# Optimization experiments

Measured on AMD Instinct MI355X. Metric: run time of the kernel, lower is better.

## Reference

```python
import jax, jax.numpy as jnp
import numpy as np


def _lstm_cell(x, h, c, Wih, Whh, b):
    # torch gate order: input, forget, cell(g), output
    gates = x @ Wih.T + h @ Whh.T + b  # [B, 4H]
    i, f, g, o = jnp.split(gates, 4, axis=-1)
    i = jax.nn.sigmoid(i)
    f = jax.nn.sigmoid(f)
    g = jnp.tanh(g)
    o = jax.nn.sigmoid(o)
    c = f * c + i * g
    return o * jnp.tanh(c), c


def setup_inputs() -> dict:
    key = jax.random.key(0)
    ks = jax.random.split(key, 20)
    B, Te, Td, X, H = 4096, 168, 24, 8, 64
    s = 0.1  # weight scale for numerical sanity in the AR sampling loop
    return {
        "enc_x": jax.random.normal(ks[0], (B, Te, X), jnp.float32),
        "enc_z": jax.random.uniform(ks[1], (B, Te, 1), jnp.float32),
        "dec_x": jax.random.normal(ks[2], (B, Td, X - 1), jnp.float32),
        "v": jax.random.uniform(ks[3], (B, 1, 1), jnp.float32) + 0.5,  # positive scale
        "eps": jax.random.normal(ks[4], (B, Td, 1), jnp.float32),
        "W_ih0": s * jax.random.normal(ks[5], (4 * H, X), jnp.float32),
        "W_hh0": s * jax.random.normal(ks[6], (4 * H, H), jnp.float32),
        "b0": s * jax.random.normal(ks[7], (4 * H,), jnp.float32),
        "W_ih1": s * jax.random.normal(ks[8], (4 * H, H), jnp.float32),
        "W_hh1": s * jax.random.normal(ks[9], (4 * H, H), jnp.float32),
        "b1": s * jax.random.normal(ks[10], (4 * H,), jnp.float32),
        "W_ih2": s * jax.random.normal(ks[11], (4 * H, H), jnp.float32),
        "W_hh2": s * jax.random.normal(ks[12], (4 * H, H), jnp.float32),
        "b2": s * jax.random.normal(ks[13], (4 * H,), jnp.float32),
        "w_m": s * jax.random.normal(ks[14], (H, 1), jnp.float32),
        "b_m": jnp.zeros((1,), jnp.float32),
        "w_a": s * jax.random.normal(ks[15], (H, 1), jnp.float32),
        "b_a": jnp.zeros((1,), jnp.float32),
    }


def reference(enc_x, enc_z, dec_x, v, eps,
              W_ih0, W_hh0, b0, W_ih1, W_hh1, b1, W_ih2, W_hh2, b2,
              w_m, b_m, w_a, b_a):
    B = enc_x.shape[0]
    H = W_hh0.shape[1]

    def step3(x, h, c):
        h0, c0 = _lstm_cell(x, h[0], c[0], W_ih0, W_hh0, b0)
        h1, c1 = _lstm_cell(h0, h[1], c[1], W_ih1, W_hh1, b1)
        h2, c2 = _lstm_cell(h1, h[2], c[2], W_ih2, W_hh2, b2)
        return (h0, h1, h2), (c0, c1, c2), h2

    z0 = jnp.zeros((B, H), enc_x.dtype)
    h = (z0, z0, z0)
    c = (z0, z0, z0)

    # ---- encoder: 3-layer LSTM over Te steps ----
    def enc_step(carry, x_t):
        h, c = carry
        h, c, _ = step3(x_t, h, c)
        return (h, c), None

    (h, c), _ = jax.lax.scan(enc_step, (h, c), jnp.swapaxes(enc_x, 0, 1))

    vf = v[:, 0, :]                 # [B, 1]
    z = enc_z[:, -1, :] / vf        # [B, 1]

    def dec_step(carry, inp):
        h, c, z = carry
        x_t, e_t = inp              # [B, X-1], [B, 1]
        x = jnp.concatenate([z, x_t], axis=-1)   # [B, X]
        h, c, o = step3(x, h, c)
        m = (o @ w_m + b_m) * vf                  # Gaussian mean, rescaled
        a = jax.nn.softplus(o @ w_a + b_a) * vf   # Gaussian std, rescaled
        zs = m + a * e_t                          # reparameterized sample
        return (h, c, zs / vf), zs

    xs = (jnp.swapaxes(dec_x, 0, 1), jnp.swapaxes(eps, 0, 1))
    _, Z = jax.lax.scan(dec_step, (h, c, z), xs)  # [Td, B, 1]
    return jnp.swapaxes(Z, 0, 1)                  # [B, Td, 1]
```

## Files before the change

kernel.cpp:

```cpp
#include <hip/hip_runtime.h>
#include <math.h>

#define B_TOT 4096
#define TE 168
#define TD 24
#define NWG 256
#define HSTR 72

typedef _Float16 f16;
typedef __attribute__((ext_vector_type(8))) _Float16 f16x8;
typedef __attribute__((ext_vector_type(4))) float f32x4;

#define SCL_S (-1.4426950408889634f)
#define SCL_G (2.885390081777927f)

__global__ __launch_bounds__(256) void pack_kernel(
    const float* __restrict__ Wih0, const float* __restrict__ Whh0,
    const float* __restrict__ Wih1, const float* __restrict__ Whh1,
    const float* __restrict__ Wih2, const float* __restrict__ Whh2,
    f16* __restrict__ pk)
{
    int idx = blockIdx.x * 256 + threadIdx.x;
    int j = idx & 7;
    int t = idx >> 3;
    int ln = t & 63; t >>= 6;
    int c  = t & 3;  t >>= 2;
    int q  = t & 3;  t >>= 2;
    int l  = t % 3;
    int w  = t / 3;
    int row = q * 64 + w * 16 + (ln & 15);
    int k   = c * 32 + ((ln >> 4) << 3) + j;
    float val = 0.f;
    if (l == 0) {
        if (k < 8)                 val = Wih0[row * 8 + k];
        else if (k >= 32 && k < 96) val = Whh0[row * 64 + (k - 32)];
    } else if (l == 1) {
        val = (k < 64) ? Wih1[row * 64 + k] : Whh1[row * 64 + (k - 64)];
    } else {
        val = (k < 64) ? Wih2[row * 64 + k] : Whh2[row * 64 + (k - 64)];
    }
    const float sc = (q == 2) ? SCL_G : SCL_S;
    pk[idx] = (f16)(val * sc);
}

__device__ __forceinline__ float softplusf(float x) { return fmaxf(x, 0.f) + log1pf(__expf(-fabsf(x))); }

__global__ __launch_bounds__(256, 1) void lstm_kernel(
    const float* __restrict__ enc_x, const float* __restrict__ enc_z,
    const float* __restrict__ dec_x, const float* __restrict__ v,
    const float* __restrict__ eps,   const f16* __restrict__ pk,
    const float* __restrict__ b0, const float* __restrict__ b1,
    const float* __restrict__ b2,
    const float* __restrict__ w_m, const float* __restrict__ b_m,
    const float* __restrict__ w_a, const float* __restrict__ b_a,
    float* __restrict__ out)
{
    const int tid  = threadIdx.x;
    const int lane = tid & 63;
    const int wv   = tid >> 6;
    const int bg   = blockIdx.x * 16;
    const int m16  = lane & 15;
    const int quad = lane >> 4;

    __shared__ f16  hbuf[2][3][16][HSTR];
    __shared__ f16  xbuf[2][16][32];
    __shared__ float zbuf[16];

    {
        uint* hz = (uint*)&hbuf[0][0][0][0];
        const int HW = 2 * 3 * 16 * HSTR / 2;
        for (int i = tid; i < HW; i += 256) hz[i] = 0u;
        uint* xz = (uint*)&xbuf[0][0][0];
        for (int i = tid; i < 512; i += 256) xz[i] = 0u;
    }

    f16x8 wgt[3][4][4];
#pragma unroll
    for (int l = 0; l < 3; ++l)
#pragma unroll
        for (int q = 0; q < 4; ++q)
#pragma unroll
            for (int c = 0; c < 4; ++c) {
                if (l == 0 && c == 3) continue;
                size_t off = (((((size_t)wv * 3 + l) * 4 + q) * 4 + c) * 64 + lane) * 8;
                wgt[l][q][c] = *(const f16x8*)(pk + off);
            }

    const int hid_self = wv * 16 + m16;
    f32x4 bsp[3][4];
#pragma unroll
    for (int q = 0; q < 4; ++q) {
        const float sc = (q == 2) ? SCL_G : SCL_S;
        float v0 = b0[q * 64 + hid_self] * sc;
        float v1 = b1[q * 64 + hid_self] * sc;
        float v2 = b2[q * 64 + hid_self] * sc;
        bsp[0][q] = (f32x4){v0, v0, v0, v0};
        bsp[1][q] = (f32x4){v1, v1, v1, v1};
        bsp[2][q] = (f32x4){v2, v2, v2, v2};
    }

    f16* hb = &hbuf[0][0][0][0];
    const int aoff = m16 * HSTR + quad * 8;
    float cst[3][4] = {};

#define HBASE(pp, l) (hb + ((pp) * 3 + (l)) * (16 * HSTR))
#define MFMA16(af, bf, cf) __builtin_amdgcn_mfma_f32_16x16x32_f16(af, bf, cf, 0, 0, 0)

#define MM_F(P, aptr, l, c)                                                   \
    {                                                                         \
        f16x8 af = *(const f16x8*)(aptr);                                     \
        P##0 = MFMA16(af, wgt[l][0][c], bsp[l][0]);                           \
        P##1 = MFMA16(af, wgt[l][1][c], bsp[l][1]);                           \
        P##2 = MFMA16(af, wgt[l][2][c], bsp[l][2]);                           \
        P##3 = MFMA16(af, wgt[l][3][c], bsp[l][3]);                           \
    }
#define MM(P, aptr, l, c)                                                     \
    {                                                                         \
        f16x8 af = *(const f16x8*)(aptr);                                     \
        P##0 = MFMA16(af, wgt[l][0][c], P##0);                                \
        P##1 = MFMA16(af, wgt[l][1][c], P##1);                                \
        P##2 = MFMA16(af, wgt[l][2][c], P##2);                                \
        P##3 = MFMA16(af, wgt[l][3][c], P##3);                                \
    }

#define CELL(P, l, PP)                                                        \
    {                                                                         \
        f16* hw = HBASE(PP, l) + hid_self;                                    \
        _Pragma("unroll")                                                     \
        for (int r = 0; r < 4; ++r) {                                         \
            float Ei = __builtin_amdgcn_exp2f(P##0[r]);                       \
            float Ef = __builtin_amdgcn_exp2f(P##1[r]);                       \
            float Eg = __builtin_amdgcn_exp2f(P##2[r]);                       \
            float Eo = __builtin_amdgcn_exp2f(P##3[r]);                       \
            float fv  = __builtin_amdgcn_rcpf(1.f + Ef);                      \
            float Rig = __builtin_amdgcn_rcpf((1.f + Ei) * (1.f + Eg));       \
            float cn  = fmaf(fv, cst[l][r], (Eg - 1.f) * Rig);                \
            cst[l][r] = cn;                                                   \
            float Ec  = __builtin_amdgcn_exp2f(cn * SCL_G);                   \
            float Roc = __builtin_amdgcn_rcpf((1.f + Eo) * (1.f + Ec));       \
            hw[(quad * 4 + r) * HSTR] = (f16)((Ec - 1.f) * Roc);              \
        }                                                                     \
    }

    const int  mS   = tid >> 3, kS = tid & 7;
    const bool isst = tid < 128;

#define ROUND(PP, D0, D1, D2, DS, DP, T0)                                     \
    {                                                                         \
        __syncthreads();                                                      \
        f32x4 a00, a01, a02, a03, a10, a11, a12, a13, a20, a21, a22, a23;     \
        if (D0) {                                                             \
            MM_F(a0, &xbuf[PP][0][0] + m16 * 32 + quad * 8, 0, 0);            \
            MM(a0, HBASE(1 - (PP), 0) + aoff,      0, 1);                     \
            MM(a0, HBASE(1 - (PP), 0) + aoff + 32, 0, 2);                     \
        }                                                                     \
        if (D1) {                                                             \
            MM_F(a1, HBASE(1 - (PP), 0) + aoff,      1, 0);                   \
            MM(a1, HBASE(1 - (PP), 0) + aoff + 32, 1, 1);                     \
            MM(a1, HBASE(1 - (PP), 1) + aoff,      1, 2);                     \
            MM(a1, HBASE(1 - (PP), 1) + aoff + 32, 1, 3);                     \
        }                                                                     \
        if (D2) {                                                             \
            MM_F(a2, HBASE(1 - (PP), 1) + aoff,      2, 0);                   \
            MM(a2, HBASE(1 - (PP), 1) + aoff + 32, 2, 1);                     \
            MM(a2, HBASE(1 - (PP), 2) + aoff,      2, 2);                     \
            MM(a2, HBASE(1 - (PP), 2) + aoff + 32, 2, 3);                     \
        }                                                                     \
        if (DS && isst) {                                                     \
            xbuf[1 - (PP)][mS][kS] = (f16)xpre;                               \
            if (DP) xpre = enc_x[((size_t)(bg + mS) * TE + (T0) + 2) * 8 + kS]; \
        }                                                                     \
        if (D0) CELL(a0, 0, PP);                                              \
        if (D1) CELL(a1, 1, PP);                                              \
        if (D2) CELL(a2, 2, PP);                                              \
    }

    __syncthreads();

    float xpre = 0.f;
    if (isst) {
        xbuf[0][mS][kS] = (f16)enc_x[((size_t)(bg + mS) * TE + 0) * 8 + kS];
        xpre = enc_x[((size_t)(bg + mS) * TE + 1) * 8 + kS];
    }
    ROUND(0, 1, 0, 0, 1, 1, 0)
    ROUND(1, 1, 1, 0, 1, 1, 1)
    for (int t = 2; t < 166; t += 2) {
        ROUND(0, 1, 1, 1, 1, 1, t)
        ROUND(1, 1, 1, 1, 1, 1, t + 1)
    }
    ROUND(0, 1, 1, 1, 1, 0, 166)
    ROUND(1, 1, 1, 1, 0, 0, 167)
    ROUND(0, 0, 1, 1, 0, 0, 168)
    ROUND(1, 0, 0, 1, 0, 0, 169)

    const int   mH = tid >> 4;
    const float vf = v[bg + mH];
    float wmr[4], war[4];
#pragma unroll
    for (int r = 0; r < 4; ++r) {
        wmr[r] = w_m[(tid & 15) + 16 * r];
        war[r] = w_a[(tid & 15) + 16 * r];
    }
    const float bmv = b_m[0], bav = b_a[0];
    if ((tid & 15) == 0) zbuf[mH] = enc_z[(size_t)(bg + mH) * TE + (TE - 1)] / vf;

#define DEC_STEP(PA, t)                                                       \
    {                                                                         \
        __syncthreads();                      \
        if (isst) {                                                           \
            float xv = (kS == 0) ? zbuf[mS]                                   \
                                 : dec_x[((size_t)(bg + mS) * TD + (t)) * 7 + (kS - 1)]; \
            xbuf[PA][mS][kS] = (f16)xv;                                       \
        }                                                                     \
        __syncthreads();                                       \
        f32x4 ac0, ac1, ac2, ac3, bc0, bc1, bc2, bc3;                         \
        MM_F(ac, &xbuf[PA][0][0] + m16 * 32 + quad * 8, 0, 0);                \
        MM_F(bc, HBASE(PA, 1) + aoff,      1, 2);                             \
        MM(ac, HBASE(1 - (PA), 0) + aoff,      0, 1);                         \
        MM(bc, HBASE(PA, 1) + aoff + 32, 1, 3);                               \
        MM(ac, HBASE(1 - (PA), 0) + aoff + 32, 0, 2);                         \
        CELL(ac, 0, PA);                                                      \
        __syncthreads();                                  \
        MM_F(ac, HBASE(1 - (PA), 2) + aoff,      2, 2);                       \
        MM(bc, HBASE(PA, 0) + aoff,      1, 0);                               \
        MM(ac, HBASE(1 - (PA), 2) + aoff + 32, 2, 3);                         \
        MM(bc, HBASE(PA, 0) + aoff + 32, 1, 1);                               \
        CELL(bc, 1, 1 - (PA));                                                \
        __syncthreads();                                \
        MM(ac, HBASE(1 - (PA), 1) + aoff,      2, 0);                         \
        MM(ac, HBASE(1 - (PA), 1) + aoff + 32, 2, 1);                         \
        CELL(ac, 2, PA);                                                      \
        __syncthreads();                                  \
        {                                                                     \
            float sm = 0.f, sa = 0.f;                                         \
            const f16* h2p = HBASE(PA, 2) + mH * HSTR;                        \
            _Pragma("unroll")                                                 \
            for (int r = 0; r < 4; ++r) {                                     \
                float hv = (float)h2p[(tid & 15) + 16 * r];                   \
                sm += hv * wmr[r];                                            \
                sa += hv * war[r];                                            \
            }                                                                 \
            _Pragma("unroll")                                                 \
            for (int off = 1; off < 16; off <<= 1) {                          \
                sm += __shfl_xor(sm, off, 64);                                \
                sa += __shfl_xor(sa, off, 64);                                \
            }                                                                 \
            if ((tid & 15) == 0) {                                            \
                float mo  = (sm + bmv) * vf;                                  \
                float ao  = softplusf(sa + bav) * vf;                         \
                float zsv = mo + ao * eps[(size_t)(bg + mH) * TD + (t)];      \
                out[(size_t)(bg + mH) * TD + (t)] = zsv;                      \
                zbuf[mH] = zsv / vf;                                          \
            }                                                                 \
        }                                                                     \
    }

    for (int t = 0; t < TD; t += 2) {
        DEC_STEP(0, t)
        DEC_STEP(1, t + 1)
    }

#undef HBASE
#undef MFMA16
#undef MM_F
#undef MM
#undef CELL
#undef ROUND
#undef DEC_STEP
}

extern "C" void kernel_launch(void* const* d_in, const int* in_sizes, int n_in,
                              void* d_out, int out_size, void* d_ws, size_t ws_size,
                              hipStream_t stream) {
    const float* enc_x = (const float*)d_in[0];
    const float* enc_z = (const float*)d_in[1];
    const float* dec_x = (const float*)d_in[2];
    const float* v     = (const float*)d_in[3];
    const float* eps   = (const float*)d_in[4];
    const float* Wih0  = (const float*)d_in[5];
    const float* Whh0  = (const float*)d_in[6];
    const float* b0    = (const float*)d_in[7];
    const float* Wih1  = (const float*)d_in[8];
    const float* Whh1  = (const float*)d_in[9];
    const float* b1    = (const float*)d_in[10];
    const float* Wih2  = (const float*)d_in[11];
    const float* Whh2  = (const float*)d_in[12];
    const float* b2    = (const float*)d_in[13];
    const float* w_m   = (const float*)d_in[14];
    const float* b_m   = (const float*)d_in[15];
    const float* w_a   = (const float*)d_in[16];
    const float* b_a   = (const float*)d_in[17];
    float* out = (float*)d_out;
    f16*   pk  = (f16*)d_ws;

    pack_kernel<<<384, 256, 0, stream>>>(Wih0, Whh0, Wih1, Whh1, Wih2, Whh2, pk);
    lstm_kernel<<<NWG, 256, 0, stream>>>(enc_x, enc_z, dec_x, v, eps, pk,
                                         b0, b1, b2, w_m, b_m, w_a, b_a, out);
}
```

Baseline: 339.1 us.

## Halve batch rows per workgroup to double workgroups and run two per CU

Each workgroup now handles 8 batch rows instead of 16, mapped into the 16-row MFMA tile via a row remap so only half the accumulator rows are real. The grid doubles and launch bounds allow two workgroups per CU, which should hide the serial recurrence latency across workgroups. Bias is moved from the MFMA accumulator init into the gate activation, and the cell math is reworked to share one reciprocal. Each cell now computes only 2 rows per lane and interleaves with the next layer's MFMAs. MFMA work per sample doubles, and register pressure must fit two workgroups.

```diff
diff --git a/kernel.cpp b/kernel.cpp
--- a/kernel.cpp
+++ b/kernel.cpp
@@ -4,7 +4,7 @@
 #define B_TOT 4096
 #define TE 168
 #define TD 24
-#define NWG 256
+#define NWG 512
 #define HSTR 72
 
 typedef _Float16 f16;
@@ -13,6 +13,8 @@
 
 #define SCL_S (-1.4426950408889634f)
 #define SCL_G (2.885390081777927f)
+
+#define RMAP(b) ((((b) >> 1) << 2) | ((b) & 1))
 
 __global__ __launch_bounds__(256) void pack_kernel(
     const float* __restrict__ Wih0, const float* __restrict__ Whh0,
@@ -45,7 +47,7 @@
 
 __device__ __forceinline__ float softplusf(float x) { return fmaxf(x, 0.f) + log1pf(__expf(-fabsf(x))); }
 
-__global__ __launch_bounds__(256, 1) void lstm_kernel(
+__global__ __launch_bounds__(256, 2) void lstm_kernel(
     const float* __restrict__ enc_x, const float* __restrict__ enc_z,
     const float* __restrict__ dec_x, const float* __restrict__ v,
     const float* __restrict__ eps,   const f16* __restrict__ pk,
@@ -58,13 +60,13 @@
     const int tid  = threadIdx.x;
     const int lane = tid & 63;
     const int wv   = tid >> 6;
-    const int bg   = blockIdx.x * 16;
+    const int bg   = blockIdx.x * 8;
     const int m16  = lane & 15;
     const int quad = lane >> 4;
 
     __shared__ f16  hbuf[2][3][16][HSTR];
     __shared__ f16  xbuf[2][16][32];
-    __shared__ float zbuf[16];
+    __shared__ float zbuf[8];
 
     {
         uint* hz = (uint*)&hbuf[0][0][0][0];
@@ -87,21 +89,19 @@
             }
 
     const int hid_self = wv * 16 + m16;
-    f32x4 bsp[3][4];
+    float bsc[3][4];
 #pragma unroll
     for (int q = 0; q < 4; ++q) {
         const float sc = (q == 2) ? SCL_G : SCL_S;
-        float v0 = b0[q * 64 + hid_self] * sc;
-        float v1 = b1[q * 64 + hid_self] * sc;
-        float v2 = b2[q * 64 + hid_self] * sc;
-        bsp[0][q] = (f32x4){v0, v0, v0, v0};
-        bsp[1][q] = (f32x4){v1, v1, v1, v1};
-        bsp[2][q] = (f32x4){v2, v2, v2, v2};
+        bsc[0][q] = b0[q * 64 + hid_self] * sc;
+        bsc[1][q] = b1[q * 64 + hid_self] * sc;
+        bsc[2][q] = b2[q * 64 + hid_self] * sc;
     }
 
     f16* hb = &hbuf[0][0][0][0];
     const int aoff = m16 * HSTR + quad * 8;
-    float cst[3][4] = {};
+    float cst[3][2] = {};
+    const f32x4 zc = {0.f, 0.f, 0.f, 0.f};
 
 #define HBASE(pp, l) (hb + ((pp) * 3 + (l)) * (16 * HSTR))
 #define MFMA16(af, bf, cf) __builtin_amdgcn_mfma_f32_16x16x32_f16(af, bf, cf, 0, 0, 0)
@@ -109,10 +109,10 @@
 #define MM_F(P, aptr, l, c)                                                   \
     {                                                                         \
         f16x8 af = *(const f16x8*)(aptr);                                     \
-        P##0 = MFMA16(af, wgt[l][0][c], bsp[l][0]);                           \
-        P##1 = MFMA16(af, wgt[l][1][c], bsp[l][1]);                           \
-        P##2 = MFMA16(af, wgt[l][2][c], bsp[l][2]);                           \
-        P##3 = MFMA16(af, wgt[l][3][c], bsp[l][3]);                           \
+        P##0 = MFMA16(af, wgt[l][0][c], zc);                                  \
+        P##1 = MFMA16(af, wgt[l][1][c], zc);                                  \
+        P##2 = MFMA16(af, wgt[l][2][c], zc);                                  \
+        P##3 = MFMA16(af, wgt[l][3][c], zc);                                  \
     }
 #define MM(P, aptr, l, c)                                                     \
     {                                                                         \
@@ -127,14 +127,17 @@
     {                                                                         \
         f16* hw = HBASE(PP, l) + hid_self;                                    \
         _Pragma("unroll")                                                     \
-        for (int r = 0; r < 4; ++r) {                                         \
-            float Ei = __builtin_amdgcn_exp2f(P##0[r]);                       \
-            float Ef = __builtin_amdgcn_exp2f(P##1[r]);                       \
-            float Eg = __builtin_amdgcn_exp2f(P##2[r]);                       \
-            float Eo = __builtin_amdgcn_exp2f(P##3[r]);                       \
-            float fv  = __builtin_amdgcn_rcpf(1.f + Ef);                      \
-            float Rig = __builtin_amdgcn_rcpf((1.f + Ei) * (1.f + Eg));       \
-            float cn  = fmaf(fv, cst[l][r], (Eg - 1.f) * Rig);                \
+        for (int r = 0; r < 2; ++r) {                                         \
+            float Ei = __builtin_amdgcn_exp2f(P##0[r] + bsc[l][0]);           \
+            float Ef = __builtin_amdgcn_exp2f(P##1[r] + bsc[l][1]);           \
+            float Eg = __builtin_amdgcn_exp2f(P##2[r] + bsc[l][2]);           \
+            float Eo = __builtin_amdgcn_exp2f(P##3[r] + bsc[l][3]);           \
+            float ef1 = 1.f + Ef;                                             \
+            float pig = (1.f + Ei) * (1.f + Eg);                              \
+            float R   = __builtin_amdgcn_rcpf(pig * ef1);                     \
+            float fv  = pig * R;                                              \
+            float ig  = (Eg - 1.f) * ef1 * R;                                 \
+            float cn  = fmaf(fv, cst[l][r], ig);                              \
             cst[l][r] = cn;                                                   \
             float Ec  = __builtin_amdgcn_exp2f(cn * SCL_G);                   \
             float Roc = __builtin_amdgcn_rcpf((1.f + Eo) * (1.f + Ec));       \
@@ -143,7 +146,9 @@
     }
 
     const int  mS   = tid >> 3, kS = tid & 7;
-    const bool isst = tid < 128;
+    const int  rmS  = RMAP(mS & 7);
+    const bool isst = tid < 64;
+    const float* xrow = enc_x + ((size_t)(bg + (mS & 7)) * TE) * 8 + kS;
 
 #define ROUND(PP, D0, D1, D2, DS, DP, T0)                                     \
     {                                                                         \
@@ -154,33 +159,33 @@
             MM(a0, HBASE(1 - (PP), 0) + aoff,      0, 1);                     \
             MM(a0, HBASE(1 - (PP), 0) + aoff + 32, 0, 2);                     \
         }                                                                     \
+        if (DS && isst) {                                                     \
+            xbuf[1 - (PP)][rmS][kS] = (f16)xpre;                              \
+            if (DP) xpre = xrow[((T0) + 2) * 8];                              \
+        }                                                                     \
+        if (D0) CELL(a0, 0, PP);                                              \
         if (D1) {                                                             \
             MM_F(a1, HBASE(1 - (PP), 0) + aoff,      1, 0);                   \
             MM(a1, HBASE(1 - (PP), 0) + aoff + 32, 1, 1);                     \
             MM(a1, HBASE(1 - (PP), 1) + aoff,      1, 2);                     \
             MM(a1, HBASE(1 - (PP), 1) + aoff + 32, 1, 3);                     \
+            CELL(a1, 1, PP);                                                  \
         }                                                                     \
         if (D2) {                                                             \
             MM_F(a2, HBASE(1 - (PP), 1) + aoff,      2, 0);                   \
             MM(a2, HBASE(1 - (PP), 1) + aoff + 32, 2, 1);                     \
             MM(a2, HBASE(1 - (PP), 2) + aoff,      2, 2);                     \
             MM(a2, HBASE(1 - (PP), 2) + aoff + 32, 2, 3);                     \
-        }                                                                     \
-        if (DS && isst) {                                                     \
-            xbuf[1 - (PP)][mS][kS] = (f16)xpre;                               \
-            if (DP) xpre = enc_x[((size_t)(bg + mS) * TE + (T0) + 2) * 8 + kS]; \
-        }                                                                     \
-        if (D0) CELL(a0, 0, PP);                                              \
-        if (D1) CELL(a1, 1, PP);                                              \
-        if (D2) CELL(a2, 2, PP);                                              \
+            CELL(a2, 2, PP);                                                  \
+        }                                                                     \
     }
 
     __syncthreads();
 
     float xpre = 0.f;
     if (isst) {
-        xbuf[0][mS][kS] = (f16)enc_x[((size_t)(bg + mS) * TE + 0) * 8 + kS];
-        xpre = enc_x[((size_t)(bg + mS) * TE + 1) * 8 + kS];
+        xbuf[0][rmS][kS] = (f16)xrow[0];
+        xpre = xrow[8];
     }
     ROUND(0, 1, 0, 0, 1, 1, 0)
     ROUND(1, 1, 1, 0, 1, 1, 1)
@@ -193,7 +198,8 @@
     ROUND(0, 0, 1, 1, 0, 0, 168)
     ROUND(1, 0, 0, 1, 0, 0, 169)
 
-    const int   mH = tid >> 4;
+    const int   mH = (tid >> 4) & 7;
+    const int   rmH = RMAP(mH);
     const float vf = v[bg + mH];
     float wmr[4], war[4];
 #pragma unroll
@@ -202,7 +208,8 @@
         war[r] = w_a[(tid & 15) + 16 * r];
     }
     const float bmv = b_m[0], bav = b_a[0];
-    if ((tid & 15) == 0) zbuf[mH] = enc_z[(size_t)(bg + mH) * TE + (TE - 1)] / vf;
+    if (tid < 128 && (tid & 15) == 0)
+        zbuf[mH] = enc_z[(size_t)(bg + mH) * TE + (TE - 1)] / vf;
 
 #define DEC_STEP(PA, t)                                                       \
     {                                                                         \
@@ -210,7 +217,7 @@
         if (isst) {                                                           \
             float xv = (kS == 0) ? zbuf[mS]                                   \
                                  : dec_x[((size_t)(bg + mS) * TD + (t)) * 7 + (kS - 1)]; \
-            xbuf[PA][mS][kS] = (f16)xv;                                       \
+            xbuf[PA][rmS][kS] = (f16)xv;                                      \
         }                                                                     \
         __syncthreads();                                       \
         f32x4 ac0, ac1, ac2, ac3, bc0, bc1, bc2, bc3;                         \
@@ -231,9 +238,9 @@
         MM(ac, HBASE(1 - (PA), 1) + aoff + 32, 2, 1);                         \
         CELL(ac, 2, PA);                                                      \
         __syncthreads();                                  \
-        {                                                                     \
+        if (tid < 128) {                                                      \
             float sm = 0.f, sa = 0.f;                                         \
-            const f16* h2p = HBASE(PA, 2) + mH * HSTR;                        \
+            const f16* h2p = HBASE(PA, 2) + rmH * HSTR;                       \
             _Pragma("unroll")                                                 \
             for (int r = 0; r < 4; ++r) {                                     \
                 float hv = (float)h2p[(tid & 15) + 16 * r];                   \
```

Result: slower. 381.8 us (+12.6%).
